# Performance work log

Measured on AMD Instinct MI355X. Metric: run time of the kernel, lower is better.

Reference implementation:

```python
import jax, jax.numpy as jnp
import numpy as np

B, C, P, NG, NCLS, HID, N, IMG = 2, 256, 7, 2, 81, 1024, 512, 800
STRIDES = [4, 8, 16, 32]
SCALE = 56.0  # roi_map_level_scale


def _roi_align(feat, rois, pooled, scale, ng):
    """torchvision-legacy (aligned=False) ROI Align. feat [B,C,H,W], rois [N,5]."""
    Bf, Cf, H, W = feat.shape
    ft = jnp.transpose(feat, (0, 2, 3, 1))  # [B,H,W,C]
    b = rois[:, 0].astype(jnp.int32)
    x1, y1, x2, y2 = (rois[:, i] * scale for i in (1, 2, 3, 4))
    rw = jnp.maximum(x2 - x1, 1.0)
    rh = jnp.maximum(y2 - y1, 1.0)
    # sample grid per output bin: ng points per axis, centered in sub-bins
    g = (jnp.arange(pooled)[:, None] + (jnp.arange(ng)[None, :] + 0.5) / ng).reshape(-1)  # [P*ng]
    ys = y1[:, None] + g[None, :] * (rh / pooled)[:, None]  # [N,S]
    xs = x1[:, None] + g[None, :] * (rw / pooled)[:, None]

    def axis(coord, size):
        valid = (coord >= -1.0) & (coord <= size)
        c = jnp.clip(coord, 0.0, size - 1)
        lo = jnp.floor(c).astype(jnp.int32)
        hi = jnp.minimum(lo + 1, size - 1)
        return valid, lo, hi, c - lo

    vy, ylo, yhi, fy = axis(ys, H)
    vx, xlo, xhi, fx = axis(xs, W)
    bb = b[:, None, None]

    def gather(yi, xi):
        return ft[bb, yi[:, :, None], xi[:, None, :], :]  # [N,S,S,C]

    wy = fy[:, :, None, None]
    wx = fx[:, None, :, None]
    val = ((1 - wy) * (1 - wx) * gather(ylo, xlo) + (1 - wy) * wx * gather(ylo, xhi)
           + wy * (1 - wx) * gather(yhi, xlo) + wy * wx * gather(yhi, xhi))
    val = jnp.where((vy[:, :, None] & vx[:, None, :])[..., None], val, 0.0)
    val = val.reshape(-1, pooled, ng, pooled, ng, Cf).mean(axis=(2, 4))  # [N,P,P,C]
    return jnp.transpose(val, (0, 3, 1, 2))  # [N,C,P,P]


def setup_inputs() -> dict:
    key = jax.random.key(0)
    ks = jax.random.split(key, 16)
    feats = {}
    for i, s in enumerate(STRIDES):
        hw = IMG // s
        feats[f"p{i+2}"] = jax.random.normal(ks[i], (B, C, hw, hw), jnp.float32)
    # realistic proposals: batch idx + boxes with sizes 16..512 px
    bidx = jax.random.randint(ks[4], (N,), 0, B).astype(jnp.float32)
    sw = 2.0 ** jax.random.uniform(ks[5], (N,), minval=4.0, maxval=9.0)
    sh = 2.0 ** jax.random.uniform(ks[6], (N,), minval=4.0, maxval=9.0)
    x1 = jax.random.uniform(ks[7], (N,)) * (IMG - sw)
    y1 = jax.random.uniform(ks[8], (N,)) * (IMG - sh)
    rois = jnp.stack([bidx, x1, y1, x1 + sw - 1, y1 + sh - 1], axis=1)
    D = C * P * P
    inp = dict(feats, rois=rois,
               w1=0.01 * jax.random.normal(ks[9], (HID, D), jnp.float32),
               b1=jnp.zeros((HID,), jnp.float32),
               w2=0.01 * jax.random.normal(ks[10], (HID, HID), jnp.float32),
               b2=jnp.zeros((HID,), jnp.float32),
               w_cls=0.01 * jax.random.normal(ks[11], (NCLS, HID), jnp.float32),
               b_cls=jnp.zeros((NCLS,), jnp.float32),
               w_reg=0.001 * jax.random.normal(ks[12], (NCLS * 4, HID), jnp.float32),
               b_reg=jnp.zeros((NCLS * 4,), jnp.float32))
    return inp


def reference(p2, p3, p4, p5, rois, w1, b1, w2, b2, w_cls, b_cls, w_reg, b_reg):
    feats = [p2, p3, p4, p5]
    # FPN level assignment (same math as torch: log2(sqrt(hw)/scale + 1e-6), floor, clamp)
    rh = rois[:, 4] - rois[:, 2] + 1
    rw = rois[:, 3] - rois[:, 1] + 1
    levels = jnp.clip(jnp.floor(jnp.log2(jnp.sqrt(rh * rw) / SCALE + 1e-6)), 0, 3).astype(jnp.int32)
    # dispatch: compute each ROI on its assigned level (masked combine == gather/sort-scatter)
    pooled = jnp.zeros((rois.shape[0], C, P, P), rois.dtype)
    for l, feat in enumerate(feats):
        pl = _roi_align(feat, rois, P, 1.0 / STRIDES[l], NG)
        pooled = pooled + jnp.where((levels == l)[:, None, None, None], pl, 0.0)
    x = pooled.reshape(pooled.shape[0], -1)  # [N, C*P*P]
    x = jax.nn.relu(x @ w1.T + b1)
    x = jax.nn.relu(x @ w2.T + b2)
    x_cls = x @ w_cls.T + b_cls
    x_reg = x @ w_reg.T + b_reg  # TEST mode, not class-agnostic: no gather
    cls_probs = jax.nn.softmax(x_cls, axis=1)
    rois_out = rois.reshape(B, -1, 5)
    cls_probs = cls_probs.reshape(B, rois_out.shape[1], -1)
    bbox_preds = x_reg.reshape(B, rois_out.shape[1], -1)
    return rois_out, cls_probs, bbox_preds
```

## Files before the change

### kernel.cpp

```cpp
#include <hip/hip_runtime.h>
#include <hip/hip_bf16.h>
#include <math.h>

#define NROI   512
#define CCH    256
#define POOLP  7
#define DDIM   12544
#define HIDN   1024
#define NCLS   81
#define NREG   324
#define NHEAD  512
#define OUT_ROIS   2560
#define OUT_CLS    (512*81)

typedef __attribute__((ext_vector_type(4))) float f32x4;
typedef __attribute__((ext_vector_type(8))) short bf16x8;

static __device__ __forceinline__ unsigned short f2bf(float x) {
    __hip_bfloat16 h = __float2bfloat16(x);
    return *reinterpret_cast<unsigned short*>(&h);
}
static __device__ __forceinline__ float bf2f(unsigned short u) {
    unsigned int b = ((unsigned int)u) << 16;
    return *reinterpret_cast<float*>(&b);
}

#define PREP_B0 10
#define PREP_B1 (PREP_B0 + 1280)
#define PREP_B2 (PREP_B1 + 1024)
#define PREP_B3 (PREP_B2 + 1024)
__global__ __launch_bounds__(256) void prep_k(const float* __restrict__ rois,
                                              const float* __restrict__ w2,
                                              const float* __restrict__ wc,
                                              const float* __restrict__ wr,
                                              float* __restrict__ out,
                                              float* __restrict__ accz,
                                              unsigned short* __restrict__ w2b,
                                              unsigned short* __restrict__ whd) {
    int bid = blockIdx.x, t = threadIdx.x;
    if (bid < PREP_B0) {
        int i = bid * 256 + t;
        if (i < OUT_ROIS) out[i] = rois[i];
    } else if (bid < PREP_B1) {
        int i = (bid - PREP_B0) * 256 + t;
        ((float4*)accz)[i] = make_float4(0.f, 0.f, 0.f, 0.f);
    } else if (bid < PREP_B2) {
        int i = (bid - PREP_B1) * 256 + t;
        float4 v = ((const float4*)w2)[i];
        ushort4 o;
        o.x = f2bf(v.x); o.y = f2bf(v.y); o.z = f2bf(v.z); o.w = f2bf(v.w);
        ((ushort4*)w2b)[i] = o;
    } else {
        int i2 = (bid - PREP_B2) * 256 + t;
        int r = i2 >> 9, c = (i2 & 511) << 1;
        float v0, v1;
        if (r < NCLS)             { v0 = wc[r * HIDN + c]; v1 = wc[r * HIDN + c + 1]; }
        else if (r < NCLS + NREG) { v0 = wr[(r - NCLS) * HIDN + c]; v1 = wr[(r - NCLS) * HIDN + c + 1]; }
        else                      { v0 = 0.f; v1 = 0.f; }
        ((unsigned int*)whd)[i2] = (unsigned int)f2bf(v0) | ((unsigned int)f2bf(v1) << 16);
    }
}

__global__ __launch_bounds__(256) void permute_w1_k(const float* __restrict__ w1,
                                                    unsigned short* __restrict__ w1b) {
    __shared__ unsigned short lw[49 * 258];
    int n = blockIdx.x, t = threadIdx.x;
    const float* src = w1 + (size_t)n * DDIM;
#pragma unroll
    for (int k = t; k < DDIM; k += 256) {
        int c = k / 49;
        int s = k - c * 49;
        lw[s * 258 + c] = f2bf(src[k]);
    }
    __syncthreads();
    unsigned int* dst = (unsigned int*)(w1b + (size_t)n * DDIM);
    for (int j2 = t; j2 < DDIM / 2; j2 += 256) {
        int s  = j2 >> 7;
        int c2 = (j2 & 127) << 1;
        dst[j2] = lw[s * 258 + c2] | ((unsigned int)lw[s * 258 + c2 + 1] << 16);
    }
}

__global__ __launch_bounds__(256) void transpose_all_k(const float* __restrict__ p2,
                                                       const float* __restrict__ p3,
                                                       const float* __restrict__ p4,
                                                       const float* __restrict__ p5,
                                                       unsigned short* __restrict__ f0,
                                                       unsigned short* __restrict__ f1,
                                                       unsigned short* __restrict__ f2,
                                                       unsigned short* __restrict__ f3) {
    __shared__ unsigned short tile[32][66];
    int xb = blockIdx.x;
    const float* in; unsigned short* outp; int S, base;
    if (xb < 1250)      { in = p2; outp = f0; S = 40000; base = 0; }
    else if (xb < 1563) { in = p3; outp = f1; S = 10000; base = 1250; }
    else if (xb < 1642) { in = p4; outp = f2; S = 2500;  base = 1563; }
    else                { in = p5; outp = f3; S = 625;   base = 1642; }
    int s0 = (xb - base) * 32;
    int c0 = blockIdx.y * 64;
    int b  = blockIdx.z;
    int t  = threadIdx.x;

    {
        int sL = t & 31, cq = t >> 5;
        const float* src = in + ((size_t)b * CCH + c0 + cq * 8) * S + s0 + sL;
        bool ok = (s0 + sL) < S;
#pragma unroll
        for (int j = 0; j < 8; j++)
            tile[sL][cq * 8 + j] = ok ? f2bf(src[(size_t)j * S]) : (unsigned short)0;
    }
    __syncthreads();
    {
        int c2 = t & 31, sq = t >> 5;
#pragma unroll
        for (int i = 0; i < 4; i++) {
            int s = sq * 4 + i;
            if (s0 + s < S) {
                unsigned int v = tile[s][c2 * 2] | ((unsigned int)tile[s][c2 * 2 + 1] << 16);
                ((unsigned int*)(outp + ((size_t)b * S + s0 + s) * CCH + c0))[c2] = v;
            }
        }
    }
}

__global__ __launch_bounds__(256) void roi_align_k(const unsigned short* __restrict__ f0,
                                                   const unsigned short* __restrict__ f1,
                                                   const unsigned short* __restrict__ f2,
                                                   const unsigned short* __restrict__ f3,
                                                   const float* __restrict__ rois,
                                                   unsigned short* __restrict__ xpool) {
    __shared__ float s_f[16];
    __shared__ int   s_lo[16], s_hi[16], s_v[16];

    int py = blockIdx.x, r = blockIdx.y, t = threadIdx.x;

    float r0  = rois[r * 5 + 0];
    float rx1 = rois[r * 5 + 1], ry1 = rois[r * 5 + 2];
    float rx2 = rois[r * 5 + 3], ry2 = rois[r * 5 + 4];
    int b = (int)r0;

    float aw = rx2 - rx1 + 1.f, ah = ry2 - ry1 + 1.f;
    float lvf = floorf(log2f(sqrtf(ah * aw) / 56.f + 1e-6f));
    int lv = (int)fminf(fmaxf(lvf, 0.f), 3.f);

    const unsigned short* F = (lv == 0) ? f0 : (lv == 1) ? f1 : (lv == 2) ? f2 : f3;
    int HW      = (lv == 0) ? 200 : (lv == 1) ? 100 : (lv == 2) ? 50 : 25;
    float scale = (lv == 0) ? 0.25f : (lv == 1) ? 0.125f : (lv == 2) ? 0.0625f : 0.03125f;

    float x1 = rx1 * scale, yy1 = ry1 * scale;
    float x2 = rx2 * scale, yy2 = ry2 * scale;
    float rw = fmaxf(x2 - x1, 1.f), rh = fmaxf(yy2 - yy1, 1.f);

    if (t < 16) {
        bool isY = t < 2;
        float coord;
        if (isY) {
            float g = (float)py + ((float)t + 0.5f) * 0.5f;
            coord = yy1 + g * (rh * (1.f / 7.f));
        } else {
            int j = t - 2;
            float g = (float)(j >> 1) + ((float)(j & 1) + 0.5f) * 0.5f;
            coord = x1 + g * (rw * (1.f / 7.f));
        }
        int vld = (coord >= -1.f && coord <= (float)HW) ? 1 : 0;
        float c = fminf(fmaxf(coord, 0.f), (float)(HW - 1));
        int lo  = (int)floorf(c);
        int hi  = min(lo + 1, HW - 1);
        s_v[t] = vld; s_lo[t] = lo; s_hi[t] = hi; s_f[t] = c - (float)lo;
    }
    __syncthreads();

    const unsigned short* Fb = F + ((size_t)b * HW * HW) * CCH + t;
    size_t obase = (size_t)r * DDIM + py * 7 * 256 + t;

    for (int px = 0; px < POOLP; px++) {
        float acc = 0.f;
#pragma unroll
        for (int s = 0; s < 4; s++) {
            int iy = s >> 1;
            int ix = px * 2 + (s & 1);
            int vy = s_v[iy], vx = s_v[2 + ix];
            if (vy & vx) {
                float fy = s_f[iy], fx = s_f[2 + ix];
                int ylo = s_lo[iy], yhi = s_hi[iy];
                int xlo = s_lo[2 + ix], xhi = s_hi[2 + ix];
                float v00 = bf2f(Fb[((size_t)ylo * HW + xlo) * CCH]);
                float v01 = bf2f(Fb[((size_t)ylo * HW + xhi) * CCH]);
                float v10 = bf2f(Fb[((size_t)yhi * HW + xlo) * CCH]);
                float v11 = bf2f(Fb[((size_t)yhi * HW + xhi) * CCH]);
                acc += (1.f - fy) * ((1.f - fx) * v00 + fx * v01)
                     + fy * ((1.f - fx) * v10 + fx * v11);
            }
        }
        xpool[obase + px * 256] = f2bf(acc * 0.25f);
    }
}

__global__ __launch_bounds__(256) void roi_align_nchw_k(const float* __restrict__ f0,
                                                        const float* __restrict__ f1,
                                                        const float* __restrict__ f2,
                                                        const float* __restrict__ f3,
                                                        const float* __restrict__ rois,
                                                        unsigned short* __restrict__ xpool) {
    __shared__ float s_f[16];
    __shared__ int   s_lo[16], s_hi[16], s_v[16];
    int py = blockIdx.x, r = blockIdx.y, t = threadIdx.x;
    float r0  = rois[r * 5 + 0];
    float rx1 = rois[r * 5 + 1], ry1 = rois[r * 5 + 2];
    float rx2 = rois[r * 5 + 3], ry2 = rois[r * 5 + 4];
    int b = (int)r0;
    float aw = rx2 - rx1 + 1.f, ah = ry2 - ry1 + 1.f;
    float lvf = floorf(log2f(sqrtf(ah * aw) / 56.f + 1e-6f));
    int lv = (int)fminf(fmaxf(lvf, 0.f), 3.f);
    const float* F = (lv == 0) ? f0 : (lv == 1) ? f1 : (lv == 2) ? f2 : f3;
    int HW      = (lv == 0) ? 200 : (lv == 1) ? 100 : (lv == 2) ? 50 : 25;
    float scale = (lv == 0) ? 0.25f : (lv == 1) ? 0.125f : (lv == 2) ? 0.0625f : 0.03125f;
    float x1 = rx1 * scale, yy1 = ry1 * scale;
    float x2 = rx2 * scale, yy2 = ry2 * scale;
    float rw = fmaxf(x2 - x1, 1.f), rh = fmaxf(yy2 - yy1, 1.f);
    if (t < 16) {
        bool isY = t < 2;
        float coord;
        if (isY) {
            float g = (float)py + ((float)t + 0.5f) * 0.5f;
            coord = yy1 + g * (rh * (1.f / 7.f));
        } else {
            int j = t - 2;
            float g = (float)(j >> 1) + ((float)(j & 1) + 0.5f) * 0.5f;
            coord = x1 + g * (rw * (1.f / 7.f));
        }
        int vld = (coord >= -1.f && coord <= (float)HW) ? 1 : 0;
        float c = fminf(fmaxf(coord, 0.f), (float)(HW - 1));
        int lo  = (int)floorf(c);
        int hi  = min(lo + 1, HW - 1);
        s_v[t] = vld; s_lo[t] = lo; s_hi[t] = hi; s_f[t] = c - (float)lo;
    }
    __syncthreads();
    const float* Fb = F + ((size_t)b * CCH + t) * HW * HW;
    size_t obase = (size_t)r * DDIM + py * 7 * 256 + t;
    for (int px = 0; px < POOLP; px++) {
        float acc = 0.f;
#pragma unroll
        for (int s = 0; s < 4; s++) {
            int iy = s >> 1, ix = px * 2 + (s & 1);
            int vy = s_v[iy], vx = s_v[2 + ix];
            if (vy & vx) {
                float fy = s_f[iy], fx = s_f[2 + ix];
                int ylo = s_lo[iy], yhi = s_hi[iy];
                int xlo = s_lo[2 + ix], xhi = s_hi[2 + ix];
                float v00 = Fb[(size_t)ylo * HW + xlo];
                float v01 = Fb[(size_t)ylo * HW + xhi];
                float v10 = Fb[(size_t)yhi * HW + xlo];
                float v11 = Fb[(size_t)yhi * HW + xhi];
                acc += (1.f - fy) * ((1.f - fx) * v00 + fx * v01)
                     + fy * ((1.f - fx) * v10 + fx * v11);
            }
        }
        xpool[obase + px * 256] = f2bf(acc * 0.25f);
    }
}

__global__ __launch_bounds__(256) void gemm_bf16_k(const unsigned short* __restrict__ A,
                                                   const unsigned short* __restrict__ W,
                                                   float* __restrict__ Cacc,
                                                   int M, int N, int K, int kchunk) {
    __shared__ __align__(16) unsigned short As[8][64][8];
    __shared__ __align__(16) unsigned short Ws[8][64][8];

    int t = threadIdx.x;
    int lane = t & 63, wid = t >> 6;
    int m0 = blockIdx.y * 64, n0 = blockIdx.x * 64;
    int k0 = blockIdx.z * kchunk;
    int wm = (wid >> 1) * 32, wn = (wid & 1) * 32;
    int fr = lane & 15, kg = lane >> 4;

    f32x4 acc[2][2] = {};

    const unsigned short* Arow = A + (size_t)(m0 + lane) * K;
    const unsigned short* Wrow = W + (size_t)(n0 + lane) * K;

    for (int kb = k0; kb < k0 + kchunk; kb += 64) {
#pragma unroll
        for (int i = 0; i < 2; i++) {
            int c = wid * 2 + i;
            __builtin_amdgcn_global_load_lds(
                (const __attribute__((address_space(1))) void*)(Arow + kb + c * 8),
                (__attribute__((address_space(3))) void*)(&As[c][0][0]), 16, 0, 0);
            __builtin_amdgcn_global_load_lds(
                (const __attribute__((address_space(1))) void*)(Wrow + kb + c * 8),
                (__attribute__((address_space(3))) void*)(&Ws[c][0][0]), 16, 0, 0);
        }
        __syncthreads();
#pragma unroll
        for (int h = 0; h < 2; h++) {
            bf16x8 a0 = *(const bf16x8*)(&As[h * 4 + kg][wm + fr][0]);
            bf16x8 a1 = *(const bf16x8*)(&As[h * 4 + kg][wm + 16 + fr][0]);
            bf16x8 b0 = *(const bf16x8*)(&Ws[h * 4 + kg][wn + fr][0]);
            bf16x8 b1 = *(const bf16x8*)(&Ws[h * 4 + kg][wn + 16 + fr][0]);
            acc[0][0] = __builtin_amdgcn_mfma_f32_16x16x32_bf16(a0, b0, acc[0][0], 0, 0, 0);
            acc[0][1] = __builtin_amdgcn_mfma_f32_16x16x32_bf16(a0, b1, acc[0][1], 0, 0, 0);
            acc[1][0] = __builtin_amdgcn_mfma_f32_16x16x32_bf16(a1, b0, acc[1][0], 0, 0, 0);
            acc[1][1] = __builtin_amdgcn_mfma_f32_16x16x32_bf16(a1, b1, acc[1][1], 0, 0, 0);
        }
        __syncthreads();
    }

    int row = m0 + wm + (lane >> 4) * 4;
    int col = n0 + wn + (lane & 15);
#pragma unroll
    for (int fm = 0; fm < 2; fm++)
#pragma unroll
        for (int fn = 0; fn < 2; fn++)
#pragma unroll
            for (int r = 0; r < 4; r++)
                atomicAdd(&Cacc[(size_t)(row + fm * 16 + r) * N + col + fn * 16],
                          acc[fm][fn][r]);
}

__global__ __launch_bounds__(256) void gemm128_bf16_k(const unsigned short* __restrict__ A,
                                                      const unsigned short* __restrict__ W,
                                                      float* __restrict__ Cacc,
                                                      int M, int N, int K, int kchunk) {
    __shared__ __align__(16) unsigned short As[8][128][8];
    __shared__ __align__(16) unsigned short Ws[8][128][8];

    int lin = blockIdx.x;
    int nb  = (lin & 7) * 56 + (lin >> 3);
    int bx = nb & 7, by = (nb >> 3) & 3, bz = nb >> 5;

    int t = threadIdx.x;
    int lane = t & 63, wid = t >> 6;
    int m0 = by * 128, n0 = bx * 128;
    int k0 = bz * kchunk;
    int wm = (wid >> 1) * 64, wn = (wid & 1) * 64;
    int fr = lane & 15, kg = lane >> 4;

    f32x4 acc[4][4] = {};

    for (int kb = k0; kb < k0 + kchunk; kb += 64) {
#pragma unroll
        for (int i = 0; i < 4; i++) {
            int c   = wid * 4 + i;
            int kgc = c >> 1;
            int r0w = (c & 1) * 64;
            __builtin_amdgcn_global_load_lds(
                (const __attribute__((address_space(1))) void*)
                    (A + (size_t)(m0 + r0w + lane) * K + kb + kgc * 8),
                (__attribute__((address_space(3))) void*)(&As[kgc][r0w][0]), 16, 0, 0);
            __builtin_amdgcn_global_load_lds(
                (const __attribute__((address_space(1))) void*)
                    (W + (size_t)(n0 + r0w + lane) * K + kb + kgc * 8),
                (__attribute__((address_space(3))) void*)(&Ws[kgc][r0w][0]), 16, 0, 0);
        }
        __syncthreads();
#pragma unroll
        for (int h = 0; h < 2; h++) {
            bf16x8 av[4], bv[4];
#pragma unroll
            for (int f = 0; f < 4; f++) {
                av[f] = *(const bf16x8*)(&As[h * 4 + kg][wm + f * 16 + fr][0]);
                bv[f] = *(const bf16x8*)(&Ws[h * 4 + kg][wn + f * 16 + fr][0]);
            }
#pragma unroll
            for (int fm = 0; fm < 4; fm++)
#pragma unroll
                for (int fn = 0; fn < 4; fn++)
                    acc[fm][fn] = __builtin_amdgcn_mfma_f32_16x16x32_bf16(
                        av[fm], bv[fn], acc[fm][fn], 0, 0, 0);
        }
        __syncthreads();
    }

    int row = m0 + wm + (lane >> 4) * 4;
    int col = n0 + wn + (lane & 15);
#pragma unroll
    for (int fm = 0; fm < 4; fm++)
#pragma unroll
        for (int fn = 0; fn < 4; fn++)
#pragma unroll
            for (int r = 0; r < 4; r++)
                atomicAdd(&Cacc[(size_t)(row + fm * 16 + r) * N + col + fn * 16],
                          acc[fm][fn][r]);
}

__global__ __launch_bounds__(256) void fc_ep_k(const float* __restrict__ acc,
                                               const float* __restrict__ bias,
                                               unsigned short* __restrict__ dst, int MN) {
    int i = blockIdx.x * 256 + threadIdx.x;
    if (i >= MN) return;
    float s = fmaxf(acc[i] + bias[i & (HIDN - 1)], 0.f);
    dst[i] = f2bf(s);
}

__global__ void head_ep_k(const float* __restrict__ hf,
                          const float* __restrict__ bc,
                          const float* __restrict__ br,
                          float* __restrict__ out) {
    int r = blockIdx.x, l = threadIdx.x;
    const float* row = hf + (size_t)r * NHEAD;

    float* reg = out + OUT_ROIS + OUT_CLS + (size_t)r * NREG;
    for (int j = l; j < NREG; j += 64) reg[j] = row[NCLS + j] + br[j];

    float v0 = row[l] + bc[l];
    float v1 = (l + 64 < NCLS) ? row[l + 64] + bc[l + 64] : -INFINITY;
    float m = fmaxf(v0, v1);
#pragma unroll
    for (int o = 32; o; o >>= 1) m = fmaxf(m, __shfl_xor(m, o));
    float e0 = __expf(v0 - m);
    float e1 = (l + 64 < NCLS) ? __expf(v1 - m) : 0.f;
    float s = e0 + e1;
#pragma unroll
    for (int o = 32; o; o >>= 1) s += __shfl_xor(s, o);
    float inv = 1.f / s;
    float* cls = out + OUT_ROIS + (size_t)r * NCLS;
    cls[l] = e0 * inv;
    if (l + 64 < NCLS) cls[l + 64] = e1 * inv;
}

extern "C" void kernel_launch(void* const* d_in, const int* in_sizes, int n_in,
                              void* d_out, int out_size, void* d_ws, size_t ws_size,
                              hipStream_t stream) {
    const float* p2   = (const float*)d_in[0];
    const float* p3   = (const float*)d_in[1];
    const float* p4   = (const float*)d_in[2];
    const float* p5   = (const float*)d_in[3];
    const float* rois = (const float*)d_in[4];
    const float* w1   = (const float*)d_in[5];
    const float* b1   = (const float*)d_in[6];
    const float* w2   = (const float*)d_in[7];
    const float* b2   = (const float*)d_in[8];
    const float* wc   = (const float*)d_in[9];
    const float* bc   = (const float*)d_in[10];
    const float* wr   = (const float*)d_in[11];
    const float* br   = (const float*)d_in[12];

    float* out = (float*)d_out;

    const int KS1 = 14;

    char* p = (char*)d_ws;
    auto alloc = [&](size_t bytes) { char* r = p; p += (bytes + 255) & ~(size_t)255; return r; };
    unsigned short* xpool = (unsigned short*)alloc((size_t)NROI * DDIM * 2);
    unsigned short* y1b   = (unsigned short*)alloc((size_t)NROI * HIDN * 2);
    unsigned short* y2b   = (unsigned short*)alloc((size_t)NROI * HIDN * 2);
    unsigned short* w1b   = (unsigned short*)alloc((size_t)HIDN * DDIM * 2);
    unsigned short* w2b   = (unsigned short*)alloc((size_t)HIDN * HIDN * 2);
    unsigned short* whd   = (unsigned short*)alloc((size_t)NHEAD * HIDN * 2);
    float*          accz  = (float*)alloc((size_t)(NROI * HIDN * 2 + NROI * NHEAD) * 4);
    unsigned short* ft0 = (unsigned short*)alloc((size_t)2 * 40000 * CCH * 2);
    unsigned short* ft1 = (unsigned short*)alloc((size_t)2 * 10000 * CCH * 2);
    unsigned short* ft2 = (unsigned short*)alloc((size_t)2 * 2500 * CCH * 2);
    unsigned short* ft3 = (unsigned short*)alloc((size_t)2 * 625 * CCH * 2);
    bool nhwc = (size_t)(p - (char*)d_ws) <= ws_size;

    float* y1f = accz;
    float* y2f = accz + (size_t)NROI * HIDN;
    float* hf  = accz + (size_t)NROI * HIDN * 2;

    prep_k<<<PREP_B3, 256, 0, stream>>>(rois, w2, wc, wr, out, accz, w2b, whd);
    permute_w1_k<<<HIDN, 256, 0, stream>>>(w1, w1b);

    if (nhwc) {
        transpose_all_k<<<dim3(1662, 4, 2), 256, 0, stream>>>(p2, p3, p4, p5,
                                                              ft0, ft1, ft2, ft3);
        roi_align_k<<<dim3(POOLP, NROI), 256, 0, stream>>>(ft0, ft1, ft2, ft3, rois, xpool);
    } else {
        roi_align_nchw_k<<<dim3(POOLP, NROI), 256, 0, stream>>>(p2, p3, p4, p5, rois, xpool);
    }

    gemm128_bf16_k<<<8 * 4 * KS1, 256, 0, stream>>>(
        xpool, w1b, y1f, NROI, HIDN, DDIM, DDIM / KS1);
    fc_ep_k<<<(NROI * HIDN + 255) / 256, 256, 0, stream>>>(y1f, b1, y1b, NROI * HIDN);

    gemm_bf16_k<<<dim3(HIDN / 64, NROI / 64, 2), 256, 0, stream>>>(
        y1b, w2b, y2f, NROI, HIDN, HIDN, HIDN / 2);
    fc_ep_k<<<(NROI * HIDN + 255) / 256, 256, 0, stream>>>(y2f, b2, y2b, NROI * HIDN);

    gemm_bf16_k<<<dim3(NHEAD / 64, NROI / 64, 4), 256, 0, stream>>>(
        y2b, whd, hf, NROI, NHEAD, HIDN, HIDN / 4);
    head_ep_k<<<NROI, 64, 0, stream>>>(hf, bc, br, out);
}
```

Baseline: 163.2 us.

## Double-buffer GEMM LDS stages and merge preprocessing kernels into one launch

Both bf16 MFMA GEMM kernels now use two LDS buffers, so the next K-slice is loaded asynchronously while the current slice is multiplied. This is meant to hide global-load latency and costs twice the shared memory per block. The weight-cast, w1-permute and feature-transpose kernels are merged into one block-indexed launch to remove launch gaps, although every block of the merged kernel now reserves the larger shared buffer. The large GEMM's block-to-tile mapping is also changed so that the K-split blocks of the same output tile are scheduled next to each other.

```diff
diff --git a/kernel.cpp b/kernel.cpp
--- a/kernel.cpp
+++ b/kernel.cpp
@@ -25,99 +25,91 @@
     return *reinterpret_cast<float*>(&b);
 }
 
-#define PREP_B0 10
-#define PREP_B1 (PREP_B0 + 1280)
-#define PREP_B2 (PREP_B1 + 1024)
-#define PREP_B3 (PREP_B2 + 1024)
-__global__ __launch_bounds__(256) void prep_k(const float* __restrict__ rois,
-                                              const float* __restrict__ w2,
-                                              const float* __restrict__ wc,
-                                              const float* __restrict__ wr,
-                                              float* __restrict__ out,
-                                              float* __restrict__ accz,
-                                              unsigned short* __restrict__ w2b,
-                                              unsigned short* __restrict__ whd) {
+#define PP_B0 10
+#define PP_B1 (PP_B0 + 1280)
+#define PP_B2 (PP_B1 + 1024)
+#define PP_B3 (PP_B2 + 1024)
+#define PP_B4 (PP_B3 + 1024)
+#define PP_B5 (PP_B4 + 13296)
+__global__ __launch_bounds__(256) void preprocess_k(
+        const float* __restrict__ rois, const float* __restrict__ w1,
+        const float* __restrict__ w2, const float* __restrict__ wc,
+        const float* __restrict__ wr,
+        const float* __restrict__ p2, const float* __restrict__ p3,
+        const float* __restrict__ p4, const float* __restrict__ p5,
+        float* __restrict__ out, float* __restrict__ accz,
+        unsigned short* __restrict__ w1b, unsigned short* __restrict__ w2b,
+        unsigned short* __restrict__ whd,
+        unsigned short* __restrict__ f0, unsigned short* __restrict__ f1,
+        unsigned short* __restrict__ f2, unsigned short* __restrict__ f3) {
+    __shared__ unsigned short sm[49 * 258];
     int bid = blockIdx.x, t = threadIdx.x;
-    if (bid < PREP_B0) {
+
+    if (bid < PP_B0) {
         int i = bid * 256 + t;
         if (i < OUT_ROIS) out[i] = rois[i];
-    } else if (bid < PREP_B1) {
-        int i = (bid - PREP_B0) * 256 + t;
+    } else if (bid < PP_B1) {
+        int i = (bid - PP_B0) * 256 + t;
         ((float4*)accz)[i] = make_float4(0.f, 0.f, 0.f, 0.f);
-    } else if (bid < PREP_B2) {
-        int i = (bid - PREP_B1) * 256 + t;
+    } else if (bid < PP_B2) {
+        int i = (bid - PP_B1) * 256 + t;
         float4 v = ((const float4*)w2)[i];
         ushort4 o;
         o.x = f2bf(v.x); o.y = f2bf(v.y); o.z = f2bf(v.z); o.w = f2bf(v.w);
         ((ushort4*)w2b)[i] = o;
-    } else {
-        int i2 = (bid - PREP_B2) * 256 + t;
+    } else if (bid < PP_B3) {
+        int i2 = (bid - PP_B2) * 256 + t;
         int r = i2 >> 9, c = (i2 & 511) << 1;
         float v0, v1;
         if (r < NCLS)             { v0 = wc[r * HIDN + c]; v1 = wc[r * HIDN + c + 1]; }
         else if (r < NCLS + NREG) { v0 = wr[(r - NCLS) * HIDN + c]; v1 = wr[(r - NCLS) * HIDN + c + 1]; }
         else                      { v0 = 0.f; v1 = 0.f; }
         ((unsigned int*)whd)[i2] = (unsigned int)f2bf(v0) | ((unsigned int)f2bf(v1) << 16);
-    }
-}
-
-__global__ __launch_bounds__(256) void permute_w1_k(const float* __restrict__ w1,
-                                                    unsigned short* __restrict__ w1b) {
-    __shared__ unsigned short lw[49 * 258];
-    int n = blockIdx.x, t = threadIdx.x;
-    const float* src = w1 + (size_t)n * DDIM;
-#pragma unroll
-    for (int k = t; k < DDIM; k += 256) {
-        int c = k / 49;
-        int s = k - c * 49;
-        lw[s * 258 + c] = f2bf(src[k]);
-    }
-    __syncthreads();
-    unsigned int* dst = (unsigned int*)(w1b + (size_t)n * DDIM);
-    for (int j2 = t; j2 < DDIM / 2; j2 += 256) {
-        int s  = j2 >> 7;
-        int c2 = (j2 & 127) << 1;
-        dst[j2] = lw[s * 258 + c2] | ((unsigned int)lw[s * 258 + c2 + 1] << 16);
-    }
-}
-
-__global__ __launch_bounds__(256) void transpose_all_k(const float* __restrict__ p2,
-                                                       const float* __restrict__ p3,
-                                                       const float* __restrict__ p4,
-                                                       const float* __restrict__ p5,
-                                                       unsigned short* __restrict__ f0,
-                                                       unsigned short* __restrict__ f1,
-                                                       unsigned short* __restrict__ f2,
-                                                       unsigned short* __restrict__ f3) {
-    __shared__ unsigned short tile[32][66];
-    int xb = blockIdx.x;
-    const float* in; unsigned short* outp; int S, base;
-    if (xb < 1250)      { in = p2; outp = f0; S = 40000; base = 0; }
-    else if (xb < 1563) { in = p3; outp = f1; S = 10000; base = 1250; }
-    else if (xb < 1642) { in = p4; outp = f2; S = 2500;  base = 1563; }
-    else                { in = p5; outp = f3; S = 625;   base = 1642; }
-    int s0 = (xb - base) * 32;
-    int c0 = blockIdx.y * 64;
-    int b  = blockIdx.z;
-    int t  = threadIdx.x;
-
-    {
-        int sL = t & 31, cq = t >> 5;
-        const float* src = in + ((size_t)b * CCH + c0 + cq * 8) * S + s0 + sL;
-        bool ok = (s0 + sL) < S;
-#pragma unroll
-        for (int j = 0; j < 8; j++)
-            tile[sL][cq * 8 + j] = ok ? f2bf(src[(size_t)j * S]) : (unsigned short)0;
-    }
-    __syncthreads();
-    {
-        int c2 = t & 31, sq = t >> 5;
-#pragma unroll
-        for (int i = 0; i < 4; i++) {
-            int s = sq * 4 + i;
-            if (s0 + s < S) {
-                unsigned int v = tile[s][c2 * 2] | ((unsigned int)tile[s][c2 * 2 + 1] << 16);
-                ((unsigned int*)(outp + ((size_t)b * S + s0 + s) * CCH + c0))[c2] = v;
+    } else if (bid < PP_B4) {
+        int n = bid - PP_B3;
+        const float* src = w1 + (size_t)n * DDIM;
+        for (int k = t; k < DDIM; k += 256) {
+            int c = k / 49;
+            int s = k - c * 49;
+            sm[s * 258 + c] = f2bf(src[k]);
+        }
+        __syncthreads();
+        unsigned int* dst = (unsigned int*)(w1b + (size_t)n * DDIM);
+        for (int j2 = t; j2 < DDIM / 2; j2 += 256) {
+            int s = j2 >> 7, c2 = (j2 & 127) << 1;
+            dst[j2] = sm[s * 258 + c2] | ((unsigned int)sm[s * 258 + c2 + 1] << 16);
+        }
+    } else {
+        int j  = bid - PP_B4;
+        int xb = j % 1662;
+        int q  = j / 1662;
+        int c0 = (q & 3) * 64;
+        int b  = q >> 2;
+        const float* in; unsigned short* op; int S, base;
+        if (xb < 1250)      { in = p2; op = f0; S = 40000; base = 0; }
+        else if (xb < 1563) { in = p3; op = f1; S = 10000; base = 1250; }
+        else if (xb < 1642) { in = p4; op = f2; S = 2500;  base = 1563; }
+        else                { in = p5; op = f3; S = 625;   base = 1642; }
+        int s0 = (xb - base) * 32;
+        {
+            int sL = t & 31, cq = t >> 5;
+            const float* src = in + ((size_t)b * CCH + c0 + cq * 8) * S + s0 + sL;
+            bool ok = (s0 + sL) < S;
+#pragma unroll
+            for (int jj = 0; jj < 8; jj++)
+                sm[sL * 66 + cq * 8 + jj] = ok ? f2bf(src[(size_t)jj * S]) : (unsigned short)0;
+        }
+        __syncthreads();
+        {
+            int c2 = t & 31, sq = t >> 5;
+#pragma unroll
+            for (int i = 0; i < 4; i++) {
+                int s = sq * 4 + i;
+                if (s0 + s < S) {
+                    unsigned int v = sm[s * 66 + c2 * 2]
+                                   | ((unsigned int)sm[s * 66 + c2 * 2 + 1] << 16);
+                    ((unsigned int*)(op + ((size_t)b * S + s0 + s) * CCH + c0))[c2] = v;
+                }
             }
         }
     }
@@ -264,8 +256,8 @@
                                                    const unsigned short* __restrict__ W,
                                                    float* __restrict__ Cacc,
                                                    int M, int N, int K, int kchunk) {
-    __shared__ __align__(16) unsigned short As[8][64][8];
-    __shared__ __align__(16) unsigned short Ws[8][64][8];
+    __shared__ __align__(16) unsigned short As[2][8][64][8];
+    __shared__ __align__(16) unsigned short Ws[2][8][64][8];
 
     int t = threadIdx.x;
     int lane = t & 63, wid = t >> 6;
@@ -273,40 +265,48 @@
     int k0 = blockIdx.z * kchunk;
     int wm = (wid >> 1) * 32, wn = (wid & 1) * 32;
     int fr = lane & 15, kg = lane >> 4;
+    int nsteps = kchunk >> 6;
 
     f32x4 acc[2][2] = {};
 
     const unsigned short* Arow = A + (size_t)(m0 + lane) * K;
     const unsigned short* Wrow = W + (size_t)(n0 + lane) * K;
 
-    for (int kb = k0; kb < k0 + kchunk; kb += 64) {
+    auto stage = [&](int buf, int kb) {
 #pragma unroll
         for (int i = 0; i < 2; i++) {
             int c = wid * 2 + i;
             __builtin_amdgcn_global_load_lds(
                 (const __attribute__((address_space(1))) void*)(Arow + kb + c * 8),
-                (__attribute__((address_space(3))) void*)(&As[c][0][0]), 16, 0, 0);
+                (__attribute__((address_space(3))) void*)(&As[buf][c][0][0]), 16, 0, 0);
             __builtin_amdgcn_global_load_lds(
                 (const __attribute__((address_space(1))) void*)(Wrow + kb + c * 8),
-                (__attribute__((address_space(3))) void*)(&Ws[c][0][0]), 16, 0, 0);
-        }
-        __syncthreads();
+                (__attribute__((address_space(3))) void*)(&Ws[buf][c][0][0]), 16, 0, 0);
+        }
+    };
+
+    stage(0, k0);
+    __syncthreads();
+    int cur = 0;
+    for (int tt = 0; tt < nsteps; ++tt) {
+        if (tt + 1 < nsteps) stage(cur ^ 1, k0 + (tt + 1) * 64);
 #pragma unroll
         for (int h = 0; h < 2; h++) {
-            bf16x8 a0 = *(const bf16x8*)(&As[h * 4 + kg][wm + fr][0]);
-            bf16x8 a1 = *(const bf16x8*)(&As[h * 4 + kg][wm + 16 + fr][0]);
-            bf16x8 b0 = *(const bf16x8*)(&Ws[h * 4 + kg][wn + fr][0]);
-            bf16x8 b1 = *(const bf16x8*)(&Ws[h * 4 + kg][wn + 16 + fr][0]);
+            bf16x8 a0 = *(const bf16x8*)(&As[cur][h * 4 + kg][wm + fr][0]);
+            bf16x8 a1 = *(const bf16x8*)(&As[cur][h * 4 + kg][wm + 16 + fr][0]);
+            bf16x8 b0 = *(const bf16x8*)(&Ws[cur][h * 4 + kg][wn + fr][0]);
+            bf16x8 b1 = *(const bf16x8*)(&Ws[cur][h * 4 + kg][wn + 16 + fr][0]);
             acc[0][0] = __builtin_amdgcn_mfma_f32_16x16x32_bf16(a0, b0, acc[0][0], 0, 0, 0);
             acc[0][1] = __builtin_amdgcn_mfma_f32_16x16x32_bf16(a0, b1, acc[0][1], 0, 0, 0);
             acc[1][0] = __builtin_amdgcn_mfma_f32_16x16x32_bf16(a1, b0, acc[1][0], 0, 0, 0);
             acc[1][1] = __builtin_amdgcn_mfma_f32_16x16x32_bf16(a1, b1, acc[1][1], 0, 0, 0);
         }
         __syncthreads();
+        cur ^= 1;
     }
 
     int row = m0 + wm + (lane >> 4) * 4;
-    int col = n0 + wn + (lane & 15);
+    int col = n0 + wn + fr;
 #pragma unroll
     for (int fm = 0; fm < 2; fm++)
 #pragma unroll
@@ -321,12 +321,13 @@
                                                       const unsigned short* __restrict__ W,
                                                       float* __restrict__ Cacc,
                                                       int M, int N, int K, int kchunk) {
-    __shared__ __align__(16) unsigned short As[8][128][8];
-    __shared__ __align__(16) unsigned short Ws[8][128][8];
-
-    int lin = blockIdx.x;
-    int nb  = (lin & 7) * 56 + (lin >> 3);
-    int bx = nb & 7, by = (nb >> 3) & 3, bz = nb >> 5;
+    __shared__ __align__(16) unsigned short As[2][8][128][8];
+    __shared__ __align__(16) unsigned short Ws[2][8][128][8];
+
+    int lin  = blockIdx.x;
+    int nb   = (lin & 7) * 56 + (lin >> 3);
+    int tile = nb / 14, bz = nb - tile * 14;
+    int bx = tile & 7, by = tile >> 3;
 
     int t = threadIdx.x;
     int lane = t & 63, wid = t >> 6;
@@ -334,10 +335,11 @@
     int k0 = bz * kchunk;
     int wm = (wid >> 1) * 64, wn = (wid & 1) * 64;
     int fr = lane & 15, kg = lane >> 4;
+    int nsteps = kchunk >> 6;
 
     f32x4 acc[4][4] = {};
 
-    for (int kb = k0; kb < k0 + kchunk; kb += 64) {
+    auto stage = [&](int buf, int kb) {
 #pragma unroll
         for (int i = 0; i < 4; i++) {
             int c   = wid * 4 + i;
@@ -346,20 +348,26 @@
             __builtin_amdgcn_global_load_lds(
                 (const __attribute__((address_space(1))) void*)
                     (A + (size_t)(m0 + r0w + lane) * K + kb + kgc * 8),
-                (__attribute__((address_space(3))) void*)(&As[kgc][r0w][0]), 16, 0, 0);
+                (__attribute__((address_space(3))) void*)(&As[buf][kgc][r0w][0]), 16, 0, 0);
             __builtin_amdgcn_global_load_lds(
                 (const __attribute__((address_space(1))) void*)
                     (W + (size_t)(n0 + r0w + lane) * K + kb + kgc * 8),
-                (__attribute__((address_space(3))) void*)(&Ws[kgc][r0w][0]), 16, 0, 0);
-        }
-        __syncthreads();
+                (__attribute__((address_space(3))) void*)(&Ws[buf][kgc][r0w][0]), 16, 0, 0);
+        }
+    };
+
+    stage(0, k0);
+    __syncthreads();
+    int cur = 0;
+    for (int tt = 0; tt < nsteps; ++tt) {
+        if (tt + 1 < nsteps) stage(cur ^ 1, k0 + (tt + 1) * 64);
 #pragma unroll
         for (int h = 0; h < 2; h++) {
             bf16x8 av[4], bv[4];
 #pragma unroll
             for (int f = 0; f < 4; f++) {
-                av[f] = *(const bf16x8*)(&As[h * 4 + kg][wm + f * 16 + fr][0]);
-                bv[f] = *(const bf16x8*)(&Ws[h * 4 + kg][wn + f * 16 + fr][0]);
+                av[f] = *(const bf16x8*)(&As[cur][h * 4 + kg][wm + f * 16 + fr][0]);
+                bv[f] = *(const bf16x8*)(&Ws[cur][h * 4 + kg][wn + f * 16 + fr][0]);
             }
 #pragma unroll
             for (int fm = 0; fm < 4; fm++)
@@ -369,10 +377,11 @@
                         av[fm], bv[fn], acc[fm][fn], 0, 0, 0);
         }
         __syncthreads();
+        cur ^= 1;
     }
 
     int row = m0 + wm + (lane >> 4) * 4;
-    int col = n0 + wn + (lane & 15);
+    int col = n0 + wn + fr;
 #pragma unroll
     for (int fm = 0; fm < 4; fm++)
 #pragma unroll
@@ -458,12 +467,11 @@
     float* y2f = accz + (size_t)NROI * HIDN;
     float* hf  = accz + (size_t)NROI * HIDN * 2;
 
-    prep_k<<<PREP_B3, 256, 0, stream>>>(rois, w2, wc, wr, out, accz, w2b, whd);
-    permute_w1_k<<<HIDN, 256, 0, stream>>>(w1, w1b);
+    preprocess_k<<<nhwc ? PP_B5 : PP_B4, 256, 0, stream>>>(
+        rois, w1, w2, wc, wr, p2, p3, p4, p5,
+        out, accz, w1b, w2b, whd, ft0, ft1, ft2, ft3);
 
     if (nhwc) {
-        transpose_all_k<<<dim3(1662, 4, 2), 256, 0, stream>>>(p2, p3, p4, p5,
-                                                              ft0, ft1, ft2, ft3);
         roi_align_k<<<dim3(POOLP, NROI), 256, 0, stream>>>(ft0, ft1, ft2, ft3, rois, xpool);
     } else {
         roi_align_nchw_k<<<dim3(POOLP, NROI), 256, 0, stream>>>(p2, p3, p4, p5, rois, xpool);
```

Measured after the change: 162.1 us. No clear change (-0.6%).
